# Kernel optimization log

Measured on AMD Instinct MI355X. Metric: run time of the kernel, lower is better.

The kernel has to match this reference:

```python
import jax, jax.numpy as jnp
import numpy as np

D = 1024
H = 16
HD = D // H
T_CTX = 2048
B = 4
EPS = 1e-5


def layer_norm(x, w, b):
    mu = jnp.mean(x, axis=-1, keepdims=True)
    var = jnp.mean(jnp.square(x - mu), axis=-1, keepdims=True)
    return (x - mu) * jax.lax.rsqrt(var + EPS) * w + b


def setup_inputs() -> dict:
    key = jax.random.key(0)
    ks = jax.random.split(key, 12)
    s_in = 1.0 / np.sqrt(D)
    s_hid = 1.0 / np.sqrt(4 * D)
    return {
        "x": jax.random.normal(ks[0], (B, T_CTX, D), dtype=jnp.float32),
        "ln1_w": jnp.ones((D,), jnp.float32),
        "ln1_b": jnp.zeros((D,), jnp.float32),
        "wq": jax.random.uniform(ks[1], (H, D, HD), jnp.float32, -s_in, s_in),
        "wk": jax.random.uniform(ks[2], (H, D, HD), jnp.float32, -s_in, s_in),
        "wv": jax.random.uniform(ks[3], (H, D, HD), jnp.float32, -s_in, s_in),
        "w_proj": jax.random.uniform(ks[4], (D, D), jnp.float32, -s_in, s_in),
        "b_proj": jax.random.uniform(ks[5], (D,), jnp.float32, -s_in, s_in),
        "ln2_w": jnp.ones((D,), jnp.float32),
        "ln2_b": jnp.zeros((D,), jnp.float32),
        "w1": jax.random.uniform(ks[6], (D, 4 * D), jnp.float32, -s_in, s_in),
        "b1": jax.random.uniform(ks[7], (4 * D,), jnp.float32, -s_in, s_in),
        "w2": jax.random.uniform(ks[8], (4 * D, D), jnp.float32, -s_hid, s_hid),
        "b2": jax.random.uniform(ks[9], (D,), jnp.float32, -s_hid, s_hid),
    }


def reference(x, ln1_w, ln1_b, wq, wk, wv, w_proj, b_proj, ln2_w, ln2_b, w1, b1, w2, b2):
    Bsz, T, C = x.shape
    # --- attention block ---
    xn = layer_norm(x, ln1_w, ln1_b)
    q = jnp.einsum('btd,hde->bhte', xn, wq)  # [B,H,T,HD]
    k = jnp.einsum('btd,hde->bhte', xn, wk)
    v = jnp.einsum('btd,hde->bhte', xn, wv)
    scores = jnp.einsum('bhte,bhse->bhts', q, k) / jnp.sqrt(jnp.float32(HD))
    causal = jnp.tril(jnp.ones((T, T), dtype=bool))
    scores = jnp.where(causal, scores, -jnp.inf)
    p = jax.nn.softmax(scores, axis=-1)  # [B,H,T,T]
    attn = jnp.einsum('bhts,bhse->bhte', p, v)
    attn = attn.transpose(0, 2, 1, 3).reshape(Bsz, T, C)  # concat heads
    x = x + attn @ w_proj + b_proj
    # --- feedforward block ---
    xn2 = layer_norm(x, ln2_w, ln2_b)
    h = jax.nn.relu(xn2 @ w1 + b1)
    x = x + h @ w2 + b2
    return x
```

## Files before the change

kernel.cpp:

```cpp
#include <hip/hip_runtime.h>


#define TCTX 2048
#define DM   1024
#define HDIM 64

typedef __attribute__((ext_vector_type(8))) __bf16 bf16x8;
typedef __attribute__((ext_vector_type(4))) float  f32x4;
typedef __attribute__((ext_vector_type(8))) unsigned short u16x8;

__device__ __forceinline__ void gload16(void* lds, const void* g) {
  __builtin_amdgcn_global_load_lds(
      (const __attribute__((address_space(1))) unsigned int*)g,
      (__attribute__((address_space(3))) unsigned int*)lds, 16, 0, 0);
}

__device__ __forceinline__ unsigned short f2bf(float f) {
  union { float f; unsigned u; } a; a.f = f;
  return (unsigned short)((a.u + 0x7fffu + ((a.u >> 16) & 1u)) >> 16);
}
__device__ __forceinline__ float bf2f(unsigned short h) {
  union { unsigned u; float f; } a; a.u = ((unsigned)h) << 16;
  return a.f;
}

__global__ __launch_bounds__(256) void ln_k(
    const float* __restrict__ in, const float* __restrict__ w,
    const float* __restrict__ b, unsigned short* __restrict__ out)
{
  const int row  = blockIdx.x * 4 + (threadIdx.x >> 6);
  const int lane = threadIdx.x & 63;
  const float* rp = in + (size_t)row * DM;
  float4 v[4];
  float s = 0.f, s2 = 0.f;
#pragma unroll
  for (int c = 0; c < 4; ++c) {
    v[c] = *reinterpret_cast<const float4*>(rp + c * 256 + lane * 4);
    s  += v[c].x + v[c].y + v[c].z + v[c].w;
    s2 += v[c].x * v[c].x + v[c].y * v[c].y + v[c].z * v[c].z + v[c].w * v[c].w;
  }
#pragma unroll
  for (int m = 1; m < 64; m <<= 1) { s += __shfl_xor(s, m, 64); s2 += __shfl_xor(s2, m, 64); }
  const float mean = s * (1.f / DM);
  const float rstd = rsqrtf(s2 * (1.f / DM) - mean * mean + 1e-5f);
#pragma unroll
  for (int c = 0; c < 4; ++c) {
    const int col = c * 256 + lane * 4;
    float4 wv = *reinterpret_cast<const float4*>(w + col);
    float4 bv = *reinterpret_cast<const float4*>(b + col);
    ushort4 o;
    o.x = f2bf((v[c].x - mean) * rstd * wv.x + bv.x);
    o.y = f2bf((v[c].y - mean) * rstd * wv.y + bv.y);
    o.z = f2bf((v[c].z - mean) * rstd * wv.z + bv.z);
    o.w = f2bf((v[c].w - mean) * rstd * wv.w + bv.w);
    *reinterpret_cast<ushort4*>(out + (size_t)row * DM + col) = o;
  }
}

__global__ __launch_bounds__(256) void ln_bf_k(
    const unsigned short* __restrict__ in, const float* __restrict__ w,
    const float* __restrict__ b, unsigned short* __restrict__ out)
{
  const int row  = blockIdx.x * 4 + (threadIdx.x >> 6);
  const int lane = threadIdx.x & 63;
  const unsigned short* rp = in + (size_t)row * DM;
  float f[16];
  float s = 0.f, s2 = 0.f;
#pragma unroll
  for (int c = 0; c < 2; ++c) {
    u16x8 v = *reinterpret_cast<const u16x8*>(rp + c * 512 + lane * 8);
#pragma unroll
    for (int j = 0; j < 8; ++j) {
      const float ff = bf2f(v[j]);
      f[c * 8 + j] = ff;
      s += ff; s2 += ff * ff;
    }
  }
#pragma unroll
  for (int m = 1; m < 64; m <<= 1) { s += __shfl_xor(s, m, 64); s2 += __shfl_xor(s2, m, 64); }
  const float mean = s * (1.f / DM);
  const float rstd = rsqrtf(s2 * (1.f / DM) - mean * mean + 1e-5f);
#pragma unroll
  for (int c = 0; c < 2; ++c) {
    const int col = c * 512 + lane * 8;
    u16x8 o;
#pragma unroll
    for (int j = 0; j < 8; j += 4) {
      float4 wv = *reinterpret_cast<const float4*>(w + col + j);
      float4 bv = *reinterpret_cast<const float4*>(b + col + j);
      o[j + 0] = f2bf((f[c * 8 + j + 0] - mean) * rstd * wv.x + bv.x);
      o[j + 1] = f2bf((f[c * 8 + j + 1] - mean) * rstd * wv.y + bv.y);
      o[j + 2] = f2bf((f[c * 8 + j + 2] - mean) * rstd * wv.z + bv.z);
      o[j + 3] = f2bf((f[c * 8 + j + 3] - mean) * rstd * wv.w + bv.w);
    }
    *reinterpret_cast<u16x8*>(out + (size_t)row * DM + col) = o;
  }
}

__global__ void tr_f32_bf16(const float* __restrict__ in, unsigned short* __restrict__ out,
                            int R, int C, long ibs, long obs)
{
  __shared__ float tile[32][33];
  in  += (size_t)blockIdx.z * ibs;
  out += (size_t)blockIdx.z * obs;
  const int c0 = blockIdx.x * 32, r0 = blockIdx.y * 32;
  for (int i = threadIdx.y; i < 32; i += 8)
    tile[i][threadIdx.x] = in[(size_t)(r0 + i) * C + c0 + threadIdx.x];
  __syncthreads();
  for (int i = threadIdx.y; i < 32; i += 8)
    out[(size_t)(c0 + i) * R + r0 + threadIdx.x] = f2bf(tile[threadIdx.x][i]);
}

__global__ void tr_v(const unsigned short* __restrict__ qkv, unsigned short* __restrict__ vt)
{
  __shared__ unsigned short tile[32][33];
  const int z = blockIdx.z, b = z >> 4, h = z & 15;
  const unsigned short* in = qkv + ((size_t)b * TCTX) * 3072 + 2048 + h * HDIM;
  unsigned short* out = vt + (size_t)z * HDIM * TCTX;
  const int c0 = blockIdx.x * 32, r0 = blockIdx.y * 32;
  for (int i = threadIdx.y; i < 32; i += 8)
    tile[i][threadIdx.x] = in[(size_t)(r0 + i) * 3072 + c0 + threadIdx.x];
  __syncthreads();
  for (int i = threadIdx.y; i < 32; i += 8)
    out[(size_t)(c0 + i) * TCTX + r0 + threadIdx.x] = tile[threadIdx.x][i];
}

template<int EPI>
__global__ __launch_bounds__(256) void gemm_k(
    const unsigned short* __restrict__ A, const unsigned short* __restrict__ Bt,
    void* __restrict__ Cp, const float* __restrict__ bias,
    const void* __restrict__ resid, int M, int N, int K)
{
  __shared__ unsigned short sA[128 * 32];
  __shared__ unsigned short sB[128 * 32];
  const int tid = threadIdx.x;
  const int bm = blockIdx.x, bn = blockIdx.y;
  const int w = tid >> 6, lane = tid & 63, lr = lane & 15, lg = lane >> 4;
  const int wm = w >> 1, wn = w & 1;

  const unsigned short* ga  = A  + (size_t)(bm * 128 + (tid >> 2)) * K + (tid & 3) * 8;
  const unsigned short* ga2 = ga + (size_t)64 * K;
  const unsigned short* gb  = Bt + (size_t)(bn * 128 + (tid >> 2)) * K + (tid & 3) * 8;
  const unsigned short* gb2 = gb + (size_t)64 * K;

  const f32x4 z4 = {0.f, 0.f, 0.f, 0.f};
  f32x4 acc[4][4];
#pragma unroll
  for (int i = 0; i < 4; ++i)
#pragma unroll
    for (int j = 0; j < 4; ++j) acc[i][j] = z4;

  const unsigned short* sAa = sA + (wm * 64 + lr) * 32 + lg * 8;
  const unsigned short* sBb = sB + (wn * 64 + lr) * 32 + lg * 8;

  for (int k0 = 0; k0 < K; k0 += 32) {
    gload16(sA + (size_t)tid * 8, ga);
    gload16(sA + (size_t)(256 + tid) * 8, ga2);
    gload16(sB + (size_t)tid * 8, gb);
    gload16(sB + (size_t)(256 + tid) * 8, gb2);
    ga += 32; ga2 += 32; gb += 32; gb2 += 32;
    __syncthreads();
    bf16x8 af[4], bfr[4];
#pragma unroll
    for (int i = 0; i < 4; ++i) af[i]  = *reinterpret_cast<const bf16x8*>(sAa + i * 512);
#pragma unroll
    for (int j = 0; j < 4; ++j) bfr[j] = *reinterpret_cast<const bf16x8*>(sBb + j * 512);
#pragma unroll
    for (int i = 0; i < 4; ++i)
#pragma unroll
      for (int j = 0; j < 4; ++j)
        acc[i][j] = __builtin_amdgcn_mfma_f32_16x16x32_bf16(af[i], bfr[j], acc[i][j], 0, 0, 0);
    __syncthreads();
  }

  const int row0 = bm * 128 + wm * 64 + lg * 4;
  const int col0 = bn * 128 + wn * 64 + lr;
#pragma unroll
  for (int i = 0; i < 4; ++i) {
#pragma unroll
    for (int j = 0; j < 4; ++j) {
      const int c = col0 + j * 16;
#pragma unroll
      for (int r = 0; r < 4; ++r) {
        const int rr = row0 + i * 16 + r;
        const size_t idx = (size_t)rr * N + c;
        const float v = acc[i][j][r];
        if constexpr (EPI == 0) {
          ((unsigned short*)Cp)[idx] = f2bf(v);
        } else if constexpr (EPI == 2) {
          const float o = v + bias[c];
          ((unsigned short*)Cp)[idx] = f2bf(o > 0.f ? o : 0.f);
        } else if constexpr (EPI == 3) {
          ((unsigned short*)Cp)[idx] = f2bf(((const float*)resid)[idx] + v + bias[c]);
        } else {
          ((float*)Cp)[idx] = bf2f(((const unsigned short*)resid)[idx]) + v + bias[c];
        }
      }
    }
  }
}

__global__ __launch_bounds__(256) void attn_k(
    const unsigned short* __restrict__ qkv, const unsigned short* __restrict__ vt,
    unsigned short* __restrict__ out)
{
  __shared__ unsigned short sK[64 * 64];
  __shared__ unsigned short sV[64 * 64];
  __shared__ unsigned short sP[4][32 * 72];

  const int qb = (int)gridDim.x - 1 - (int)blockIdx.x;
  const int z = blockIdx.y, b = z >> 4, h = z & 15;
  const int tid = threadIdx.x;
  const int wv_ = tid >> 6, lane = tid & 63, lr = lane & 15, lg = lane >> 4;
  const int q_lo = qb * 128 + wv_ * 32;

  bf16x8 qf[2][2];
#pragma unroll
  for (int mt = 0; mt < 2; ++mt)
#pragma unroll
    for (int kk = 0; kk < 2; ++kk)
      qf[mt][kk] = *reinterpret_cast<const bf16x8*>(
          qkv + ((size_t)(b * TCTX + q_lo + mt * 16 + lr)) * 3072 + h * HDIM + kk * 32 + lg * 8);

  const f32x4 z4 = {0.f, 0.f, 0.f, 0.f};
  f32x4 accO[2][4];
  float rm[2][4], rl[2][4];
#pragma unroll
  for (int mt = 0; mt < 2; ++mt) {
#pragma unroll
    for (int et = 0; et < 4; ++et) accO[mt][et] = z4;
#pragma unroll
    for (int r = 0; r < 4; ++r) { rm[mt][r] = -1e30f; rl[mt][r] = 0.f; }
  }

  const int srow = tid >> 3, sch = tid & 7;
  const int sc1 = sch ^ (srow & 7);
  unsigned short* sPw = sP[wv_];

  const int nkv = 2 * qb + 2;
  for (int t = 0; t < nkv; ++t) {
    const int kvb = t * 64;
    __syncthreads();
    gload16(sK + (size_t)tid * 8,
            qkv + ((size_t)(b * TCTX + kvb + srow)) * 3072 + 1024 + h * HDIM + sc1 * 8);
    gload16(sK + (size_t)(256 + tid) * 8,
            qkv + ((size_t)(b * TCTX + kvb + 32 + srow)) * 3072 + 1024 + h * HDIM + sc1 * 8);
    gload16(sV + (size_t)tid * 8,
            vt + ((size_t)(z * 64 + srow)) * TCTX + kvb + sc1 * 8);
    gload16(sV + (size_t)(256 + tid) * 8,
            vt + ((size_t)(z * 64 + 32 + srow)) * TCTX + kvb + sc1 * 8);
    __syncthreads();
    if (kvb > q_lo + 31) continue;

    f32x4 accS[2][4];
#pragma unroll
    for (int mt = 0; mt < 2; ++mt)
#pragma unroll
      for (int nt = 0; nt < 4; ++nt) accS[mt][nt] = z4;
#pragma unroll
    for (int nt = 0; nt < 4; ++nt) {
      const int krow = nt * 16 + lr;
#pragma unroll
      for (int kk = 0; kk < 2; ++kk) {
        const int boff = ((krow * 64 + kk * 32 + lg * 8) * 2) ^ ((krow & 7) << 4);
        bf16x8 kf = *reinterpret_cast<const bf16x8*>((const char*)sK + boff);
        accS[0][nt] = __builtin_amdgcn_mfma_f32_16x16x32_bf16(qf[0][kk], kf, accS[0][nt], 0, 0, 0);
        accS[1][nt] = __builtin_amdgcn_mfma_f32_16x16x32_bf16(qf[1][kk], kf, accS[1][nt], 0, 0, 0);
      }
    }
#pragma unroll
    for (int mt = 0; mt < 2; ++mt) {
#pragma unroll
      for (int r = 0; r < 4; ++r) {
        const int q = q_lo + mt * 16 + lg * 4 + r;
        float mx = -1e30f;
#pragma unroll
        for (int nt = 0; nt < 4; ++nt) {
          float sv = accS[mt][nt][r] * 0.125f;
          if (kvb + nt * 16 + lr > q) sv = -1e30f;
          accS[mt][nt][r] = sv;
          mx = fmaxf(mx, sv);
        }
#pragma unroll
        for (int m = 1; m < 16; m <<= 1) mx = fmaxf(mx, __shfl_xor(mx, m, 64));
        const float mo = rm[mt][r];
        const float mn = fmaxf(mo, mx);
        const float sf = __expf(mo - mn);
        float rs = 0.f;
#pragma unroll
        for (int nt = 0; nt < 4; ++nt) {
          const float p = __expf(accS[mt][nt][r] - mn);
          rs += p;
          sPw[(mt * 16 + lg * 4 + r) * 72 + nt * 16 + lr] = f2bf(p);
        }
#pragma unroll
        for (int m = 1; m < 16; m <<= 1) rs += __shfl_xor(rs, m, 64);
        rm[mt][r] = mn;
        rl[mt][r] = rl[mt][r] * sf + rs;
#pragma unroll
        for (int et = 0; et < 4; ++et) accO[mt][et][r] *= sf;
      }
    }
#pragma unroll
    for (int kk = 0; kk < 2; ++kk) {
      bf16x8 pa0 = *reinterpret_cast<const bf16x8*>(sPw + (0 * 16 + lr) * 72 + kk * 32 + lg * 8);
      bf16x8 pa1 = *reinterpret_cast<const bf16x8*>(sPw + (1 * 16 + lr) * 72 + kk * 32 + lg * 8);
#pragma unroll
      for (int et = 0; et < 4; ++et) {
        const int vrow = et * 16 + lr;
        const int boff = ((vrow * 64 + kk * 32 + lg * 8) * 2) ^ ((vrow & 7) << 4);
        bf16x8 vf = *reinterpret_cast<const bf16x8*>((const char*)sV + boff);
        accO[0][et] = __builtin_amdgcn_mfma_f32_16x16x32_bf16(pa0, vf, accO[0][et], 0, 0, 0);
        accO[1][et] = __builtin_amdgcn_mfma_f32_16x16x32_bf16(pa1, vf, accO[1][et], 0, 0, 0);
      }
    }
  }
#pragma unroll
  for (int mt = 0; mt < 2; ++mt)
#pragma unroll
    for (int r = 0; r < 4; ++r) {
      const int q = q_lo + mt * 16 + lg * 4 + r;
      const float inv = 1.f / rl[mt][r];
#pragma unroll
      for (int et = 0; et < 4; ++et)
        out[((size_t)(b * TCTX + q)) * DM + h * HDIM + et * 16 + lr] =
            f2bf(accO[mt][et][r] * inv);
    }
}

extern "C" void kernel_launch(void* const* d_in, const int* in_sizes, int n_in,
                              void* d_out, int out_size, void* d_ws, size_t ws_size,
                              hipStream_t stream)
{
  const float* x     = (const float*)d_in[0];
  const float* ln1w  = (const float*)d_in[1];
  const float* ln1b  = (const float*)d_in[2];
  const float* wq    = (const float*)d_in[3];
  const float* wk    = (const float*)d_in[4];
  const float* wvp   = (const float*)d_in[5];
  const float* wproj = (const float*)d_in[6];
  const float* bproj = (const float*)d_in[7];
  const float* ln2w  = (const float*)d_in[8];
  const float* ln2b  = (const float*)d_in[9];
  const float* w1    = (const float*)d_in[10];
  const float* b1    = (const float*)d_in[11];
  const float* w2    = (const float*)d_in[12];
  const float* b2    = (const float*)d_in[13];

  char* ws = (char*)d_ws;
  unsigned short* xn     = (unsigned short*)(ws + 0);
  unsigned short* qkvb   = (unsigned short*)(ws + 16777216);
  unsigned short* vtb    = (unsigned short*)(ws + 67108864);
  unsigned short* ybf    = (unsigned short*)(ws + 83886080);
  unsigned short* wqkvT  = (unsigned short*)(ws + 100663296);
  unsigned short* wprojT = (unsigned short*)(ws + 106954752);
  unsigned short* w1T    = (unsigned short*)(ws + 109051904);
  unsigned short* w2T    = (unsigned short*)(ws + 117440512);
  unsigned short* attnb  = xn;
  unsigned short* xn2    = xn;
  unsigned short* hb     = qkvb;

  dim3 tb(32, 8);
  tr_f32_bf16<<<dim3(2, 32, 16), tb, 0, stream>>>(wq,  wqkvT,               1024, 64, 65536, 65536);
  tr_f32_bf16<<<dim3(2, 32, 16), tb, 0, stream>>>(wk,  wqkvT + 1024 * 1024, 1024, 64, 65536, 65536);
  tr_f32_bf16<<<dim3(2, 32, 16), tb, 0, stream>>>(wvp, wqkvT + 2048 * 1024, 1024, 64, 65536, 65536);
  tr_f32_bf16<<<dim3(32, 32, 1),  tb, 0, stream>>>(wproj, wprojT, 1024, 1024, 0, 0);
  tr_f32_bf16<<<dim3(128, 32, 1), tb, 0, stream>>>(w1, w1T, 1024, 4096, 0, 0);
  tr_f32_bf16<<<dim3(32, 128, 1), tb, 0, stream>>>(w2, w2T, 4096, 1024, 0, 0);

  ln_k<<<2048, 256, 0, stream>>>(x, ln1w, ln1b, xn);
  gemm_k<0><<<dim3(64, 24), 256, 0, stream>>>(xn, wqkvT, qkvb, nullptr, nullptr, 8192, 3072, 1024);
  tr_v<<<dim3(2, 64, 64), tb, 0, stream>>>(qkvb, vtb);
  attn_k<<<dim3(16, 64), 256, 0, stream>>>(qkvb, vtb, attnb);
  gemm_k<3><<<dim3(64, 8), 256, 0, stream>>>(attnb, wprojT, ybf, bproj, x, 8192, 1024, 1024);
  ln_bf_k<<<2048, 256, 0, stream>>>(ybf, ln2w, ln2b, xn2);
  gemm_k<2><<<dim3(64, 32), 256, 0, stream>>>(xn2, w1T, hb, b1, nullptr, 8192, 4096, 1024);
  gemm_k<4><<<dim3(64, 8), 256, 0, stream>>>(hb, w2T, d_out, b2, ybf, 8192, 1024, 4096);
}
```

Before: 721.1 us.

## Double-buffer K/V tiles and pair causal query blocks per attention workgroup

The attention kernel now keeps two LDS buffers for K and V and issues the next tile's async global-to-LDS loads before computing on the current one. This hides load latency and removes one barrier per iteration. Each workgroup also processes two query blocks (qb and 15-qb), which balances causal work and halves the grid to 8x64. MFMA sections are wrapped in s_setprio to favour matrix issue. LDS use doubles for K/V, and the smaller grid means fewer workgroups to spread across CUs.

```diff
diff --git a/kernel.cpp b/kernel.cpp
--- a/kernel.cpp
+++ b/kernel.cpp
@@ -204,128 +204,146 @@
     const unsigned short* __restrict__ qkv, const unsigned short* __restrict__ vt,
     unsigned short* __restrict__ out)
 {
-  __shared__ unsigned short sK[64 * 64];
-  __shared__ unsigned short sV[64 * 64];
+  __shared__ unsigned short sK[2][64 * 64];
+  __shared__ unsigned short sV[2][64 * 64];
   __shared__ unsigned short sP[4][32 * 72];
 
-  const int qb = (int)gridDim.x - 1 - (int)blockIdx.x;
   const int z = blockIdx.y, b = z >> 4, h = z & 15;
   const int tid = threadIdx.x;
   const int wv_ = tid >> 6, lane = tid & 63, lr = lane & 15, lg = lane >> 4;
-  const int q_lo = qb * 128 + wv_ * 32;
-
-  bf16x8 qf[2][2];
-#pragma unroll
-  for (int mt = 0; mt < 2; ++mt)
-#pragma unroll
-    for (int kk = 0; kk < 2; ++kk)
-      qf[mt][kk] = *reinterpret_cast<const bf16x8*>(
-          qkv + ((size_t)(b * TCTX + q_lo + mt * 16 + lr)) * 3072 + h * HDIM + kk * 32 + lg * 8);
-
-  const f32x4 z4 = {0.f, 0.f, 0.f, 0.f};
-  f32x4 accO[2][4];
-  float rm[2][4], rl[2][4];
-#pragma unroll
-  for (int mt = 0; mt < 2; ++mt) {
-#pragma unroll
-    for (int et = 0; et < 4; ++et) accO[mt][et] = z4;
-#pragma unroll
-    for (int r = 0; r < 4; ++r) { rm[mt][r] = -1e30f; rl[mt][r] = 0.f; }
-  }
-
   const int srow = tid >> 3, sch = tid & 7;
   const int sc1 = sch ^ (srow & 7);
   unsigned short* sPw = sP[wv_];
 
-  const int nkv = 2 * qb + 2;
-  for (int t = 0; t < nkv; ++t) {
-    const int kvb = t * 64;
+  const unsigned short* kbase =
+      qkv + ((size_t)(b * TCTX + srow)) * 3072 + 1024 + h * HDIM + sc1 * 8;
+  const unsigned short* vbase = vt + ((size_t)(z * 64 + srow)) * TCTX + sc1 * 8;
+
+#define STAGE(buf, kvb) do {                                                  \
+    gload16(sK[buf] + (size_t)tid * 8,         kbase + (size_t)(kvb) * 3072); \
+    gload16(sK[buf] + (size_t)(256 + tid) * 8, kbase + (size_t)((kvb) + 32) * 3072); \
+    gload16(sV[buf] + (size_t)tid * 8,         vbase + (kvb));                \
+    gload16(sV[buf] + (size_t)(256 + tid) * 8, vbase + 32 * TCTX + (kvb));    \
+  } while (0)
+
+  const f32x4 z4 = {0.f, 0.f, 0.f, 0.f};
+
+  for (int half = 0; half < 2; ++half) {
+    const int qb = (half == 0) ? (15 - (int)blockIdx.x) : (int)blockIdx.x;
+    const int q_lo = qb * 128 + wv_ * 32;
+
+    bf16x8 qf[2][2];
+#pragma unroll
+    for (int mt = 0; mt < 2; ++mt)
+#pragma unroll
+      for (int kk = 0; kk < 2; ++kk)
+        qf[mt][kk] = *reinterpret_cast<const bf16x8*>(
+            qkv + ((size_t)(b * TCTX + q_lo + mt * 16 + lr)) * 3072 + h * HDIM + kk * 32 + lg * 8);
+
+    f32x4 accO[2][4];
+    float rm[2][4], rl[2][4];
+#pragma unroll
+    for (int mt = 0; mt < 2; ++mt) {
+#pragma unroll
+      for (int et = 0; et < 4; ++et) accO[mt][et] = z4;
+#pragma unroll
+      for (int r = 0; r < 4; ++r) { rm[mt][r] = -1e30f; rl[mt][r] = 0.f; }
+    }
+
+    const int nkv = 2 * qb + 2;
+    int cur = 0;
+    STAGE(0, 0);
     __syncthreads();
-    gload16(sK + (size_t)tid * 8,
-            qkv + ((size_t)(b * TCTX + kvb + srow)) * 3072 + 1024 + h * HDIM + sc1 * 8);
-    gload16(sK + (size_t)(256 + tid) * 8,
-            qkv + ((size_t)(b * TCTX + kvb + 32 + srow)) * 3072 + 1024 + h * HDIM + sc1 * 8);
-    gload16(sV + (size_t)tid * 8,
-            vt + ((size_t)(z * 64 + srow)) * TCTX + kvb + sc1 * 8);
-    gload16(sV + (size_t)(256 + tid) * 8,
-            vt + ((size_t)(z * 64 + 32 + srow)) * TCTX + kvb + sc1 * 8);
-    __syncthreads();
-    if (kvb > q_lo + 31) continue;
-
-    f32x4 accS[2][4];
+
+    for (int t = 0; t < nkv; ++t) {
+      const int kvb = t * 64;
+      if (t + 1 < nkv) STAGE(cur ^ 1, kvb + 64);
+      if (kvb <= q_lo + 31) {
+        const unsigned short* sKc = sK[cur];
+        const unsigned short* sVc = sV[cur];
+        f32x4 accS[2][4];
+#pragma unroll
+        for (int mt = 0; mt < 2; ++mt)
+#pragma unroll
+          for (int nt = 0; nt < 4; ++nt) accS[mt][nt] = z4;
+        __builtin_amdgcn_s_setprio(1);
+#pragma unroll
+        for (int nt = 0; nt < 4; ++nt) {
+          const int krow = nt * 16 + lr;
+#pragma unroll
+          for (int kk = 0; kk < 2; ++kk) {
+            const int boff = ((krow * 64 + kk * 32 + lg * 8) * 2) ^ ((krow & 7) << 4);
+            bf16x8 kf = *reinterpret_cast<const bf16x8*>((const char*)sKc + boff);
+            accS[0][nt] = __builtin_amdgcn_mfma_f32_16x16x32_bf16(qf[0][kk], kf, accS[0][nt], 0, 0, 0);
+            accS[1][nt] = __builtin_amdgcn_mfma_f32_16x16x32_bf16(qf[1][kk], kf, accS[1][nt], 0, 0, 0);
+          }
+        }
+        __builtin_amdgcn_s_setprio(0);
+#pragma unroll
+        for (int mt = 0; mt < 2; ++mt) {
+#pragma unroll
+          for (int r = 0; r < 4; ++r) {
+            const int q = q_lo + mt * 16 + lg * 4 + r;
+            float mx = -1e30f;
+#pragma unroll
+            for (int nt = 0; nt < 4; ++nt) {
+              float sv = accS[mt][nt][r] * 0.125f;
+              if (kvb + nt * 16 + lr > q) sv = -1e30f;
+              accS[mt][nt][r] = sv;
+              mx = fmaxf(mx, sv);
+            }
+#pragma unroll
+            for (int m = 1; m < 16; m <<= 1) mx = fmaxf(mx, __shfl_xor(mx, m, 64));
+            const float mo = rm[mt][r];
+            const float mn = fmaxf(mo, mx);
+            const float sf = __expf(mo - mn);
+            float rs = 0.f;
+#pragma unroll
+            for (int nt = 0; nt < 4; ++nt) {
+              const float p = __expf(accS[mt][nt][r] - mn);
+              rs += p;
+              sPw[(mt * 16 + lg * 4 + r) * 72 + nt * 16 + lr] = f2bf(p);
+            }
+#pragma unroll
+            for (int m = 1; m < 16; m <<= 1) rs += __shfl_xor(rs, m, 64);
+            rm[mt][r] = mn;
+            rl[mt][r] = rl[mt][r] * sf + rs;
+#pragma unroll
+            for (int et = 0; et < 4; ++et) accO[mt][et][r] *= sf;
+          }
+        }
+        __builtin_amdgcn_s_setprio(1);
+#pragma unroll
+        for (int kk = 0; kk < 2; ++kk) {
+          bf16x8 pa0 = *reinterpret_cast<const bf16x8*>(sPw + (0 * 16 + lr) * 72 + kk * 32 + lg * 8);
+          bf16x8 pa1 = *reinterpret_cast<const bf16x8*>(sPw + (1 * 16 + lr) * 72 + kk * 32 + lg * 8);
+#pragma unroll
+          for (int et = 0; et < 4; ++et) {
+            const int vrow = et * 16 + lr;
+            const int boff = ((vrow * 64 + kk * 32 + lg * 8) * 2) ^ ((vrow & 7) << 4);
+            bf16x8 vf = *reinterpret_cast<const bf16x8*>((const char*)sVc + boff);
+            accO[0][et] = __builtin_amdgcn_mfma_f32_16x16x32_bf16(pa0, vf, accO[0][et], 0, 0, 0);
+            accO[1][et] = __builtin_amdgcn_mfma_f32_16x16x32_bf16(pa1, vf, accO[1][et], 0, 0, 0);
+          }
+        }
+        __builtin_amdgcn_s_setprio(0);
+      }
+      __syncthreads();
+      cur ^= 1;
+    }
 #pragma unroll
     for (int mt = 0; mt < 2; ++mt)
-#pragma unroll
-      for (int nt = 0; nt < 4; ++nt) accS[mt][nt] = z4;
-#pragma unroll
-    for (int nt = 0; nt < 4; ++nt) {
-      const int krow = nt * 16 + lr;
-#pragma unroll
-      for (int kk = 0; kk < 2; ++kk) {
-        const int boff = ((krow * 64 + kk * 32 + lg * 8) * 2) ^ ((krow & 7) << 4);
-        bf16x8 kf = *reinterpret_cast<const bf16x8*>((const char*)sK + boff);
-        accS[0][nt] = __builtin_amdgcn_mfma_f32_16x16x32_bf16(qf[0][kk], kf, accS[0][nt], 0, 0, 0);
-        accS[1][nt] = __builtin_amdgcn_mfma_f32_16x16x32_bf16(qf[1][kk], kf, accS[1][nt], 0, 0, 0);
-      }
-    }
-#pragma unroll
-    for (int mt = 0; mt < 2; ++mt) {
 #pragma unroll
       for (int r = 0; r < 4; ++r) {
         const int q = q_lo + mt * 16 + lg * 4 + r;
-        float mx = -1e30f;
-#pragma unroll
-        for (int nt = 0; nt < 4; ++nt) {
-          float sv = accS[mt][nt][r] * 0.125f;
-          if (kvb + nt * 16 + lr > q) sv = -1e30f;
-          accS[mt][nt][r] = sv;
-          mx = fmaxf(mx, sv);
-        }
-#pragma unroll
-        for (int m = 1; m < 16; m <<= 1) mx = fmaxf(mx, __shfl_xor(mx, m, 64));
-        const float mo = rm[mt][r];
-        const float mn = fmaxf(mo, mx);
-        const float sf = __expf(mo - mn);
-        float rs = 0.f;
-#pragma unroll
-        for (int nt = 0; nt < 4; ++nt) {
-          const float p = __expf(accS[mt][nt][r] - mn);
-          rs += p;
-          sPw[(mt * 16 + lg * 4 + r) * 72 + nt * 16 + lr] = f2bf(p);
-        }
-#pragma unroll
-        for (int m = 1; m < 16; m <<= 1) rs += __shfl_xor(rs, m, 64);
-        rm[mt][r] = mn;
-        rl[mt][r] = rl[mt][r] * sf + rs;
-#pragma unroll
-        for (int et = 0; et < 4; ++et) accO[mt][et][r] *= sf;
+        const float inv = 1.f / rl[mt][r];
+#pragma unroll
+        for (int et = 0; et < 4; ++et)
+          out[((size_t)(b * TCTX + q)) * DM + h * HDIM + et * 16 + lr] =
+              f2bf(accO[mt][et][r] * inv);
       }
-    }
-#pragma unroll
-    for (int kk = 0; kk < 2; ++kk) {
-      bf16x8 pa0 = *reinterpret_cast<const bf16x8*>(sPw + (0 * 16 + lr) * 72 + kk * 32 + lg * 8);
-      bf16x8 pa1 = *reinterpret_cast<const bf16x8*>(sPw + (1 * 16 + lr) * 72 + kk * 32 + lg * 8);
-#pragma unroll
-      for (int et = 0; et < 4; ++et) {
-        const int vrow = et * 16 + lr;
-        const int boff = ((vrow * 64 + kk * 32 + lg * 8) * 2) ^ ((vrow & 7) << 4);
-        bf16x8 vf = *reinterpret_cast<const bf16x8*>((const char*)sV + boff);
-        accO[0][et] = __builtin_amdgcn_mfma_f32_16x16x32_bf16(pa0, vf, accO[0][et], 0, 0, 0);
-        accO[1][et] = __builtin_amdgcn_mfma_f32_16x16x32_bf16(pa1, vf, accO[1][et], 0, 0, 0);
-      }
-    }
-  }
-#pragma unroll
-  for (int mt = 0; mt < 2; ++mt)
-#pragma unroll
-    for (int r = 0; r < 4; ++r) {
-      const int q = q_lo + mt * 16 + lg * 4 + r;
-      const float inv = 1.f / rl[mt][r];
-#pragma unroll
-      for (int et = 0; et < 4; ++et)
-        out[((size_t)(b * TCTX + q)) * DM + h * HDIM + et * 16 + lr] =
-            f2bf(accO[mt][et][r] * inv);
-    }
+  }
+#undef STAGE
 }
 
 extern "C" void kernel_launch(void* const* d_in, const int* in_sizes, int n_in,
@@ -371,7 +389,7 @@
   ln_k<<<2048, 256, 0, stream>>>(x, ln1w, ln1b, xn);
   gemm_k<0><<<dim3(64, 24), 256, 0, stream>>>(xn, wqkvT, qkvb, nullptr, nullptr, 8192, 3072, 1024);
   tr_v<<<dim3(2, 64, 64), tb, 0, stream>>>(qkvb, vtb);
-  attn_k<<<dim3(16, 64), 256, 0, stream>>>(qkvb, vtb, attnb);
+  attn_k<<<dim3(8, 64), 256, 0, stream>>>(qkvb, vtb, attnb);
   gemm_k<3><<<dim3(64, 8), 256, 0, stream>>>(attnb, wprojT, ybf, bproj, x, 8192, 1024, 1024);
   ln_bf_k<<<2048, 256, 0, stream>>>(ybf, ln2w, ln2b, xn2);
   gemm_k<2><<<dim3(64, 32), 256, 0, stream>>>(xn2, w1T, hb, b1, nullptr, 8192, 4096, 1024);
```

Measured after the change: 595.6 us. 1.21x faster.
